# Optimization experiments

Measured on AMD Instinct MI355X. Metric: run time of the kernel, lower is better.

The kernel has to match this reference:

```python
import jax, jax.numpy as jnp
import numpy as np

PAD_IDX = 0
LABEL_SMOOTHING = 0.1
END_WEIGHT = 3.0
CHAR_WEIGHT = 0.2
LENGTH_PENALTY = 0.1
B, S, V = 512, 128, 1024


def setup_inputs() -> dict:
    key = jax.random.key(0)
    k1, k2 = jax.random.split(key)
    output = jax.random.normal(k1, (B, S, V), dtype=jnp.float32)
    target = jax.random.randint(k2, (B, S), 0, V, dtype=jnp.int32)
    return {"output": output, "target": target}


def _position_weights(target):
    # weights[i, :L] = 1 + (pos/L)*0.5 ; last 3 valid positions get end-char boosts
    mask = target != PAD_IDX
    L = mask.sum(axis=1)                      # [B] int
    pos = jnp.arange(target.shape[1])[None, :]  # [1, S]
    Lc = L[:, None]
    Lf = jnp.maximum(Lc, 1).astype(jnp.float32)
    w = jnp.where(pos < Lc, 1.0 + (pos.astype(jnp.float32) / Lf) * 0.5, 1.0)
    w = jnp.where((pos == Lc - 3) & (Lc >= 3), END_WEIGHT * 0.6, w)
    w = jnp.where((pos == Lc - 2) & (Lc >= 2), END_WEIGHT * 0.8, w)
    w = jnp.where((pos == Lc - 1) & (Lc >= 1), END_WEIGHT, w)
    return w


def reference(output, target):
    Bn, Sn, Vn = output.shape
    pad_mask = target != PAD_IDX

    # label-smoothed CE, reduction='none', ignore_index=PAD_IDX
    logp = jax.nn.log_softmax(output, axis=-1)                       # [B,S,V]
    nll = -jnp.take_along_axis(logp, target[..., None], axis=-1)[..., 0]
    smooth = -jnp.mean(logp, axis=-1)
    ce = (1.0 - LABEL_SMOOTHING) * nll + LABEL_SMOOTHING * smooth
    ce = jnp.where(pad_mask, ce, 0.0)                                # [B,S]

    weights = _position_weights(target)
    weighted_loss = (ce * weights).sum() / weights.sum()

    # length penalty (argmax-based, zero-grad in original too)
    pred = jnp.argmax(output, axis=-1)                               # [B,S]
    pred_len = (pred != PAD_IDX).sum(axis=1)
    tgt_len = pad_mask.sum(axis=1)
    length_penalty = LENGTH_PENALTY * jnp.mean(
        jnp.abs(pred_len.astype(jnp.float32) - tgt_len.astype(jnp.float32)))

    # char n-gram MSE without materializing [B,S,V] one-hots:
    # onehot(a)*onehot(b) is nonzero (==1 at index a) iff a==b. For such indicator
    # tensors p,t: sum_v (p-t)^2 = p_on + t_on - 2*(p_on & t_on & same_index).
    f32 = jnp.float32
    pe = pred[:, :-1] == pred[:, 1:]          # pred bigram on
    te = target[:, :-1] == target[:, 1:]      # target bigram on
    same = pred[:, :-1] == target[:, :-1]     # same active vocab index
    bi_sq = pe.astype(f32) + te.astype(f32) - 2.0 * (pe & te & same).astype(f32)
    bigram_mse = bi_sq.sum() / (Bn * (Sn - 1) * Vn)

    pe3 = pe[:, :-1] & (pred[:, 1:-1] == pred[:, 2:])
    te3 = te[:, :-1] & (target[:, 1:-1] == target[:, 2:])
    tri_sq = pe3.astype(f32) + te3.astype(f32) - 2.0 * (pe3 & te3 & same[:, :-1]).astype(f32)
    tri_mse = tri_sq.sum() / (Bn * (Sn - 2) * Vn)
    valid_tri = jnp.any(pad_mask[:, :-2].sum(axis=1) > 0)
    char_ngram_loss = bigram_mse + jnp.where(valid_tri, tri_mse, 0.0)

    total_loss = weighted_loss + length_penalty + CHAR_WEIGHT * char_ngram_loss

    # metrics (no-grad in original)
    correct = (pred == target) & pad_mask
    total_chars = pad_mask.sum().astype(f32)
    char_acc = jnp.where(total_chars > 0, correct.sum().astype(f32) / total_chars, 0.0)
    end_idx = jnp.clip(tgt_len - 1, 0, Sn - 1)
    rows = jnp.arange(Bn)
    end_ok = (pred[rows, end_idx] == target[rows, end_idx]) & (tgt_len > 0)
    end_char_acc = end_ok.sum().astype(f32) / Bn
    length_acc = (tgt_len == pred_len).astype(f32).mean()

    return (total_loss, char_acc, end_char_acc, length_acc)
```

## Files before the change

kernel.cpp:

```cpp
#include <hip/hip_runtime.h>
#include <hip/hip_bf16.h>
#include <math.h>

#define BB 512
#define SS 128
#define VV 1024
#define NROWS (BB * SS)
#define PAD_IDX 0

#define OFF_CE    0
#define OFF_PRED  262144
#define OFF_FAC   524288
#define OFF_IAC   524352

__global__ void zero_acc(float* fac, int* iac) {
    int i = threadIdx.x;
    if (i < 2) fac[i] = 0.0f;
    if (i < 8) iac[i] = 0;
}

__global__ __launch_bounds__(256) void row_kernel(
    const float* __restrict__ logits, const int* __restrict__ tgt,
    float* __restrict__ ce, int* __restrict__ pred)
{
    const int wave = threadIdx.x >> 6;
    const int lane = threadIdx.x & 63;
    const int row  = blockIdx.x * 4 + wave;
    const float* base = logits + (size_t)row * VV;

    float4 v[4];
#pragma unroll
    for (int j = 0; j < 4; ++j)
        v[j] = reinterpret_cast<const float4*>(base)[j * 64 + lane];

    float m = -INFINITY; int am = VV;
#pragma unroll
    for (int j = 0; j < 4; ++j) {
        const int idx0 = j * 256 + lane * 4;
        float xs[4] = {v[j].x, v[j].y, v[j].z, v[j].w};
#pragma unroll
        for (int k = 0; k < 4; ++k) {
            float x = xs[k]; int idx = idx0 + k;
            if (x > m || (x == m && idx < am)) { m = x; am = idx; }
        }
    }
#pragma unroll
    for (int off = 32; off > 0; off >>= 1) {
        float om = __shfl_xor(m, off, 64);
        int   oa = __shfl_xor(am, off, 64);
        if (om > m || (om == m && oa < am)) { m = om; am = oa; }
    }

    const int t = tgt[row];

    float se = 0.0f, sx = 0.0f, xt = 0.0f;
#pragma unroll
    for (int j = 0; j < 4; ++j) {
        const int idx0 = j * 256 + lane * 4;
        float xs[4] = {v[j].x, v[j].y, v[j].z, v[j].w};
#pragma unroll
        for (int k = 0; k < 4; ++k) {
            float x = xs[k];
            se += __expf(x - m);
            sx += x;
            if (idx0 + k == t) xt = x;
        }
    }
#pragma unroll
    for (int off = 32; off > 0; off >>= 1) {
        se += __shfl_xor(se, off, 64);
        sx += __shfl_xor(sx, off, 64);
        xt += __shfl_xor(xt, off, 64);
    }

    if (lane == 0) {
        float lse    = m + __logf(se);
        float nll    = lse - xt;
        float smooth = lse - sx * (1.0f / (float)VV);
        float c = (t != PAD_IDX) ? (0.9f * nll + 0.1f * smooth) : 0.0f;
        ce[row]   = c;
        pred[row] = am;
    }
}

__global__ __launch_bounds__(128) void batch_kernel(
    const int* __restrict__ tgt, const float* __restrict__ ce,
    const int* __restrict__ pred, float* __restrict__ fac, int* __restrict__ iac)
{
    const int b = blockIdx.x;
    const int s = threadIdx.x;
    const int wave = s >> 6, lane = s & 63;

    __shared__ int sh_t[SS], sh_p[SS];
    __shared__ int sL[2], sPL[2], sCor[2], sFront[2];
    __shared__ float sRW[2], sRCW[2];
    __shared__ int sRBi[2], sRTri[2];

    const int   t = tgt[b * SS + s];
    const int   p = pred[b * SS + s];
    const float c = ce[b * SS + s];
    sh_t[s] = t; sh_p[s] = p;

    unsigned long long bal;
    bal = __ballot(t != PAD_IDX);              if (!lane) sL[wave]     = __popcll(bal);
    bal = __ballot(p != PAD_IDX);              if (!lane) sPL[wave]    = __popcll(bal);
    bal = __ballot(p == t && t != PAD_IDX);    if (!lane) sCor[wave]   = __popcll(bal);
    bal = __ballot(t != PAD_IDX && s < SS-2);  if (!lane) sFront[wave] = __popcll(bal);
    __syncthreads();

    const int L    = sL[0] + sL[1];
    const int plen = sPL[0] + sPL[1];

    float Lf = fmaxf((float)L, 1.0f);
    float w  = (s < L) ? 1.0f + ((float)s / Lf) * 0.5f : 1.0f;
    if (s == L - 3 && L >= 3) w = 3.0f * 0.6f;
    if (s == L - 2 && L >= 2) w = 3.0f * 0.8f;
    if (s == L - 1 && L >= 1) w = 3.0f;
    float cw = c * w;

    int bi = 0, tri = 0;
    if (s < SS - 1) {
        int pe = (p == sh_p[s + 1]);
        int te = (t == sh_t[s + 1]);
        int sm = (p == t);
        bi = pe + te - 2 * (pe & te & sm);
        if (s < SS - 2) {
            int pe3 = pe & (sh_p[s + 1] == sh_p[s + 2]);
            int te3 = te & (sh_t[s + 1] == sh_t[s + 2]);
            tri = pe3 + te3 - 2 * (pe3 & te3 & sm);
        }
    }

    float rw = w, rcw = cw; int rbi = bi, rtri = tri;
#pragma unroll
    for (int off = 32; off > 0; off >>= 1) {
        rw  += __shfl_xor(rw,  off, 64);
        rcw += __shfl_xor(rcw, off, 64);
        rbi += __shfl_xor(rbi, off, 64);
        rtri+= __shfl_xor(rtri,off, 64);
    }
    if (!lane) { sRW[wave] = rw; sRCW[wave] = rcw; sRBi[wave] = rbi; sRTri[wave] = rtri; }
    __syncthreads();

    if (s == 0) {
        float sumw  = sRW[0]  + sRW[1];
        float sumcw = sRCW[0] + sRCW[1];
        int bis  = sRBi[0]  + sRBi[1];
        int tris = sRTri[0] + sRTri[1];
        int cor  = sCor[0]  + sCor[1];
        int front= sFront[0]+ sFront[1];

        int end_idx = L - 1; if (end_idx < 0) end_idx = 0; if (end_idx > SS-1) end_idx = SS-1;
        int eok = (L > 0) && (sh_p[end_idx] == sh_t[end_idx]);

        atomicAdd(&fac[0], sumcw);
        atomicAdd(&fac[1], sumw);
        int d = plen - L; if (d < 0) d = -d;
        atomicAdd(&iac[0], d);
        atomicAdd(&iac[1], bis);
        atomicAdd(&iac[2], tris);
        atomicAdd(&iac[3], cor);
        atomicAdd(&iac[4], L);
        atomicAdd(&iac[5], eok ? 1 : 0);
        atomicAdd(&iac[6], (L == plen) ? 1 : 0);
        if (front > 0) atomicOr(&iac[7], 1);
    }
}

__global__ void finalize(const float* __restrict__ fac, const int* __restrict__ iac,
                         float* __restrict__ out)
{
    if (threadIdx.x == 0 && blockIdx.x == 0) {
        float weighted = fac[0] / fac[1];
        float lp  = 0.1f * (float)iac[0] / (float)BB;
        float bi  = (float)iac[1] / ((float)BB * (float)(SS - 1) * (float)VV);
        float tri = (float)iac[2] / ((float)BB * (float)(SS - 2) * (float)VV);
        float cng = bi + (iac[7] ? tri : 0.0f);
        out[0] = weighted + lp + 0.2f * cng;
        out[1] = iac[4] > 0 ? (float)iac[3] / (float)iac[4] : 0.0f;
        out[2] = (float)iac[5] / (float)BB;
        out[3] = (float)iac[6] / (float)BB;
    }
}

extern "C" void kernel_launch(void* const* d_in, const int* in_sizes, int n_in,
                              void* d_out, int out_size, void* d_ws, size_t ws_size,
                              hipStream_t stream)
{
    const float* logits = (const float*)d_in[0];
    const int*   tgt    = (const int*)d_in[1];
    float* out = (float*)d_out;

    char* ws = (char*)d_ws;
    float* ce   = (float*)(ws + OFF_CE);
    int*   pred = (int*)  (ws + OFF_PRED);
    float* fac  = (float*)(ws + OFF_FAC);
    int*   iac  = (int*)  (ws + OFF_IAC);

    zero_acc<<<1, 64, 0, stream>>>(fac, iac);
    row_kernel<<<NROWS / 4, 256, 0, stream>>>(logits, tgt, ce, pred);
    batch_kernel<<<BB, SS, 0, stream>>>(tgt, ce, pred, fac, iac);
    finalize<<<1, 1, 0, stream>>>(fac, iac, out);
}
```

Measured before the change: 410.1 us.

## Persistent row waves with next-row prefetch, shuffle target gather, fused finalize

The row kernel now launches a fixed grid where each wave processes several rows, prefetching the next row's logits into registers while it reduces the current one. Max and argmax are computed separately, with argmax taken as the lowest index equal to the max. The target logit is fetched with a single lane shuffle instead of a per-element compare. The finalize kernel is folded into the batch kernel through a last-block counter, and the zero kernel is replaced by a memset, which removes launches but adds register pressure and a threadfence.

```diff
diff --git a/kernel.cpp b/kernel.cpp
--- a/kernel.cpp
+++ b/kernel.cpp
@@ -1,5 +1,4 @@
 #include <hip/hip_runtime.h>
-#include <hip/hip_bf16.h>
 #include <math.h>
 
 #define BB 512
@@ -8,84 +7,91 @@
 #define NROWS (BB * SS)
 #define PAD_IDX 0
 
-#define OFF_CE    0
-#define OFF_PRED  262144
-#define OFF_FAC   524288
-#define OFF_IAC   524352
-
-__global__ void zero_acc(float* fac, int* iac) {
-    int i = threadIdx.x;
-    if (i < 2) fac[i] = 0.0f;
-    if (i < 8) iac[i] = 0;
-}
+#define NBLK 2048
+#define WPB  4
+#define NWAVES (NBLK * WPB)
+#define RPW (NROWS / NWAVES)
+
+#define OFF_CE   0
+#define OFF_PRED 262144
+#define OFF_ACC  524288
 
 __global__ __launch_bounds__(256) void row_kernel(
     const float* __restrict__ logits, const int* __restrict__ tgt,
     float* __restrict__ ce, int* __restrict__ pred)
 {
-    const int wave = threadIdx.x >> 6;
     const int lane = threadIdx.x & 63;
-    const int row  = blockIdx.x * 4 + wave;
-    const float* base = logits + (size_t)row * VV;
-
-    float4 v[4];
-#pragma unroll
-    for (int j = 0; j < 4; ++j)
-        v[j] = reinterpret_cast<const float4*>(base)[j * 64 + lane];
-
-    float m = -INFINITY; int am = VV;
-#pragma unroll
-    for (int j = 0; j < 4; ++j) {
-        const int idx0 = j * 256 + lane * 4;
-        float xs[4] = {v[j].x, v[j].y, v[j].z, v[j].w};
-#pragma unroll
-        for (int k = 0; k < 4; ++k) {
-            float x = xs[k]; int idx = idx0 + k;
-            if (x > m || (x == m && idx < am)) { m = x; am = idx; }
-        }
-    }
-#pragma unroll
-    for (int off = 32; off > 0; off >>= 1) {
-        float om = __shfl_xor(m, off, 64);
-        int   oa = __shfl_xor(am, off, 64);
-        if (om > m || (om == m && oa < am)) { m = om; am = oa; }
-    }
-
-    const int t = tgt[row];
-
-    float se = 0.0f, sx = 0.0f, xt = 0.0f;
-#pragma unroll
-    for (int j = 0; j < 4; ++j) {
-        const int idx0 = j * 256 + lane * 4;
-        float xs[4] = {v[j].x, v[j].y, v[j].z, v[j].w};
-#pragma unroll
-        for (int k = 0; k < 4; ++k) {
-            float x = xs[k];
-            se += __expf(x - m);
-            sx += x;
-            if (idx0 + k == t) xt = x;
-        }
-    }
-#pragma unroll
-    for (int off = 32; off > 0; off >>= 1) {
-        se += __shfl_xor(se, off, 64);
-        sx += __shfl_xor(sx, off, 64);
-        xt += __shfl_xor(xt, off, 64);
-    }
-
-    if (lane == 0) {
-        float lse    = m + __logf(se);
-        float nll    = lse - xt;
-        float smooth = lse - sx * (1.0f / (float)VV);
-        float c = (t != PAD_IDX) ? (0.9f * nll + 0.1f * smooth) : 0.0f;
-        ce[row]   = c;
-        pred[row] = am;
+    const int wid  = blockIdx.x * WPB + (threadIdx.x >> 6);
+    const int row0 = wid * RPW;
+
+    float4 cur[4], nxt[4];
+    const float4* p0 = reinterpret_cast<const float4*>(logits + (size_t)row0 * VV);
+#pragma unroll
+    for (int j = 0; j < 4; ++j) cur[j] = p0[j * 64 + lane];
+    int t = tgt[row0];
+
+    for (int i = 0; i < RPW; ++i) {
+        const int row = row0 + i;
+        int tn = 0;
+        if (i + 1 < RPW) {
+            const float4* pn = reinterpret_cast<const float4*>(logits + (size_t)(row + 1) * VV);
+#pragma unroll
+            for (int j = 0; j < 4; ++j) nxt[j] = pn[j * 64 + lane];
+            tn = tgt[row + 1];
+        }
+
+        float m = -INFINITY;
+#pragma unroll
+        for (int j = 0; j < 4; ++j)
+            m = fmaxf(m, fmaxf(fmaxf(cur[j].x, cur[j].y), fmaxf(cur[j].z, cur[j].w)));
+#pragma unroll
+        for (int off = 32; off > 0; off >>= 1)
+            m = fmaxf(m, __shfl_xor(m, off, 64));
+
+        float se = 0.0f, sx = 0.0f;
+        int am = 0x7fffffff;
+#pragma unroll
+        for (int j = 0; j < 4; ++j) {
+            float xs[4] = {cur[j].x, cur[j].y, cur[j].z, cur[j].w};
+#pragma unroll
+            for (int k = 0; k < 4; ++k) {
+                float x = xs[k];
+                int idx = j * 256 + lane * 4 + k;
+                sx += x;
+                se += __expf(x - m);
+                if (x == m) am = min(am, idx);
+            }
+        }
+
+        const int jt = t >> 8, lt = (t >> 2) & 63, kt = t & 3;
+        float4 vj = (jt == 0) ? cur[0] : (jt == 1) ? cur[1] : (jt == 2) ? cur[2] : cur[3];
+        float xc  = (kt == 0) ? vj.x : (kt == 1) ? vj.y : (kt == 2) ? vj.z : vj.w;
+        float xt  = __shfl(xc, lt, 64);
+
+#pragma unroll
+        for (int off = 32; off > 0; off >>= 1) {
+            se += __shfl_xor(se, off, 64);
+            sx += __shfl_xor(sx, off, 64);
+            am = min(am, __shfl_xor(am, off, 64));
+        }
+
+        if (lane == 0) {
+            float lse    = m + __logf(se);
+            float nll    = lse - xt;
+            float smooth = lse - sx * (1.0f / (float)VV);
+            ce[row]   = (t != PAD_IDX) ? (0.9f * nll + 0.1f * smooth) : 0.0f;
+            pred[row] = am;
+        }
+
+#pragma unroll
+        for (int j = 0; j < 4; ++j) cur[j] = nxt[j];
+        t = tn;
     }
 }
 
 __global__ __launch_bounds__(128) void batch_kernel(
     const int* __restrict__ tgt, const float* __restrict__ ce,
-    const int* __restrict__ pred, float* __restrict__ fac, int* __restrict__ iac)
+    const int* __restrict__ pred, float* fac, int* iac, float* out)
 {
     const int b = blockIdx.x;
     const int s = threadIdx.x;
@@ -102,10 +108,10 @@
     sh_t[s] = t; sh_p[s] = p;
 
     unsigned long long bal;
-    bal = __ballot(t != PAD_IDX);              if (!lane) sL[wave]     = __popcll(bal);
-    bal = __ballot(p != PAD_IDX);              if (!lane) sPL[wave]    = __popcll(bal);
-    bal = __ballot(p == t && t != PAD_IDX);    if (!lane) sCor[wave]   = __popcll(bal);
-    bal = __ballot(t != PAD_IDX && s < SS-2);  if (!lane) sFront[wave] = __popcll(bal);
+    bal = __ballot(t != PAD_IDX);               if (!lane) sL[wave]     = __popcll(bal);
+    bal = __ballot(p != PAD_IDX);               if (!lane) sPL[wave]    = __popcll(bal);
+    bal = __ballot(p == t && t != PAD_IDX);     if (!lane) sCor[wave]   = __popcll(bal);
+    bal = __ballot(t != PAD_IDX && s < SS - 2); if (!lane) sFront[wave] = __popcll(bal);
     __syncthreads();
 
     const int L    = sL[0] + sL[1];
@@ -113,8 +119,8 @@
 
     float Lf = fmaxf((float)L, 1.0f);
     float w  = (s < L) ? 1.0f + ((float)s / Lf) * 0.5f : 1.0f;
-    if (s == L - 3 && L >= 3) w = 3.0f * 0.6f;
-    if (s == L - 2 && L >= 2) w = 3.0f * 0.8f;
+    if (s == L - 3 && L >= 3) w = 1.8f;
+    if (s == L - 2 && L >= 2) w = 2.4f;
     if (s == L - 1 && L >= 1) w = 3.0f;
     float cw = c * w;
 
@@ -134,23 +140,23 @@
     float rw = w, rcw = cw; int rbi = bi, rtri = tri;
 #pragma unroll
     for (int off = 32; off > 0; off >>= 1) {
-        rw  += __shfl_xor(rw,  off, 64);
-        rcw += __shfl_xor(rcw, off, 64);
-        rbi += __shfl_xor(rbi, off, 64);
-        rtri+= __shfl_xor(rtri,off, 64);
+        rw   += __shfl_xor(rw,   off, 64);
+        rcw  += __shfl_xor(rcw,  off, 64);
+        rbi  += __shfl_xor(rbi,  off, 64);
+        rtri += __shfl_xor(rtri, off, 64);
     }
     if (!lane) { sRW[wave] = rw; sRCW[wave] = rcw; sRBi[wave] = rbi; sRTri[wave] = rtri; }
     __syncthreads();
 
     if (s == 0) {
-        float sumw  = sRW[0]  + sRW[1];
+        float sumw  = sRW[0] + sRW[1];
         float sumcw = sRCW[0] + sRCW[1];
-        int bis  = sRBi[0]  + sRBi[1];
-        int tris = sRTri[0] + sRTri[1];
-        int cor  = sCor[0]  + sCor[1];
-        int front= sFront[0]+ sFront[1];
-
-        int end_idx = L - 1; if (end_idx < 0) end_idx = 0; if (end_idx > SS-1) end_idx = SS-1;
+        int bis   = sRBi[0]  + sRBi[1];
+        int tris  = sRTri[0] + sRTri[1];
+        int cor   = sCor[0]  + sCor[1];
+        int front = sFront[0] + sFront[1];
+
+        int end_idx = L - 1; if (end_idx < 0) end_idx = 0; if (end_idx > SS - 1) end_idx = SS - 1;
         int eok = (L > 0) && (sh_p[end_idx] == sh_t[end_idx]);
 
         atomicAdd(&fac[0], sumcw);
@@ -164,22 +170,22 @@
         atomicAdd(&iac[5], eok ? 1 : 0);
         atomicAdd(&iac[6], (L == plen) ? 1 : 0);
         if (front > 0) atomicOr(&iac[7], 1);
-    }
-}
-
-__global__ void finalize(const float* __restrict__ fac, const int* __restrict__ iac,
-                         float* __restrict__ out)
-{
-    if (threadIdx.x == 0 && blockIdx.x == 0) {
-        float weighted = fac[0] / fac[1];
-        float lp  = 0.1f * (float)iac[0] / (float)BB;
-        float bi  = (float)iac[1] / ((float)BB * (float)(SS - 1) * (float)VV);
-        float tri = (float)iac[2] / ((float)BB * (float)(SS - 2) * (float)VV);
-        float cng = bi + (iac[7] ? tri : 0.0f);
-        out[0] = weighted + lp + 0.2f * cng;
-        out[1] = iac[4] > 0 ? (float)iac[3] / (float)iac[4] : 0.0f;
-        out[2] = (float)iac[5] / (float)BB;
-        out[3] = (float)iac[6] / (float)BB;
+
+        __threadfence();
+        int done = atomicAdd(&iac[9], 1);
+        if (done == BB - 1) {
+            volatile float* vf = fac;
+            volatile int*   vi = iac;
+            float weighted = vf[0] / vf[1];
+            float lp   = 0.1f * (float)vi[0] / (float)BB;
+            float bif  = (float)vi[1] / ((float)BB * (float)(SS - 1) * (float)VV);
+            float trif = (float)vi[2] / ((float)BB * (float)(SS - 2) * (float)VV);
+            float cng  = bif + (vi[7] ? trif : 0.0f);
+            out[0] = weighted + lp + 0.2f * cng;
+            out[1] = vi[4] > 0 ? (float)vi[3] / (float)vi[4] : 0.0f;
+            out[2] = (float)vi[5] / (float)BB;
+            out[3] = (float)vi[6] / (float)BB;
+        }
     }
 }
 
@@ -194,11 +200,10 @@
     char* ws = (char*)d_ws;
     float* ce   = (float*)(ws + OFF_CE);
     int*   pred = (int*)  (ws + OFF_PRED);
-    float* fac  = (float*)(ws + OFF_FAC);
-    int*   iac  = (int*)  (ws + OFF_IAC);
-
-    zero_acc<<<1, 64, 0, stream>>>(fac, iac);
-    row_kernel<<<NROWS / 4, 256, 0, stream>>>(logits, tgt, ce, pred);
-    batch_kernel<<<BB, SS, 0, stream>>>(tgt, ce, pred, fac, iac);
-    finalize<<<1, 1, 0, stream>>>(fac, iac, out);
+    float* fac  = (float*)(ws + OFF_ACC);
+    int*   iac  = (int*)  (ws + OFF_ACC + 8);
+
+    hipMemsetAsync(ws + OFF_ACC, 0, 64, stream);
+    row_kernel<<<NBLK, 256, 0, stream>>>(logits, tgt, ce, pred);
+    batch_kernel<<<BB, SS, 0, stream>>>(tgt, ce, pred, fac, iac, out);
 }
```

Result: slower. 454.8 us (+10.9%).
